# Optimization experiments

Hardware: AMD Instinct MI355X
Metric: run time of the kernel (lower is better)

Reference implementation:

```python
import jax, jax.numpy as jnp
import numpy as np

D_IN = 1024
D_OUT = 1024
NUM_HEADS = 16
HEAD_DIM = D_OUT // NUM_HEADS


def setup_inputs() -> dict:
    key = jax.random.key(0)
    ks = jax.random.split(key, 6)
    s = 0.02
    return {
        "x": jax.random.normal(ks[0], (4, 2048, D_IN), dtype=jnp.float32),
        "W_q": jax.random.normal(ks[1], (D_IN, D_OUT), dtype=jnp.float32) * s,
        "W_k": jax.random.normal(ks[2], (D_IN, D_OUT), dtype=jnp.float32) * s,
        "W_v": jax.random.normal(ks[3], (D_IN, D_OUT), dtype=jnp.float32) * s,
        "W_o": jax.random.normal(ks[4], (D_OUT, D_OUT), dtype=jnp.float32) * s,
        "b_o": jax.random.normal(ks[5], (D_OUT,), dtype=jnp.float32) * s,
    }


def reference(x, W_q, W_k, W_v, W_o, b_o):
    b, n, _ = x.shape
    # project and split heads: [b, h, n, d]
    q = (x @ W_q).reshape(b, n, NUM_HEADS, HEAD_DIM).transpose(0, 2, 1, 3)
    k = (x @ W_k).reshape(b, n, NUM_HEADS, HEAD_DIM).transpose(0, 2, 1, 3)
    v = (x @ W_v).reshape(b, n, NUM_HEADS, HEAD_DIM).transpose(0, 2, 1, 3)
    scores = jnp.einsum("bhqd,bhkd->bhqk", q, k)
    causal = jnp.tril(jnp.ones((n, n), dtype=bool))  # True = keep
    scores = jnp.where(causal, scores, -jnp.inf)
    attn = jax.nn.softmax(scores / np.sqrt(HEAD_DIM).astype(np.float32), axis=-1)
    ctx = jnp.einsum("bhqk,bhkd->bhqd", attn, v)
    ctx = ctx.transpose(0, 2, 1, 3).reshape(b, n, D_OUT)
    return ctx @ W_o + b_o
```

## Files before the change

### kernel.cpp

```cpp
#include <hip/hip_runtime.h>
#include <hip/hip_bf16.h>

#define NHEADS 16
#define HDIM 64
#define SEQ 2048
#define BATCH 4
#define DMODEL 1024
#define MTOT (BATCH * SEQ)

typedef short v8s __attribute__((ext_vector_type(8)));
typedef short v4s __attribute__((ext_vector_type(4)));
typedef float v4f __attribute__((ext_vector_type(4)));
typedef unsigned short u16;
typedef unsigned int u32;

__device__ __forceinline__ u16 f2bf(float f) {
    union { float f; unsigned u; } v; v.f = f;
    unsigned r = v.u + 0x7FFFu + ((v.u >> 16) & 1u);
    return (u16)(r >> 16);
}

__device__ __forceinline__ void g2l16(const u16* g, short* l) {
    __builtin_amdgcn_global_load_lds(
        (const __attribute__((address_space(1))) u32*)g,
        (__attribute__((address_space(3))) u32*)l, 16, 0, 0);
}

__global__ __launch_bounds__(256)
void xcvt(const float* __restrict__ x, u16* __restrict__ xb)
{
    size_t i = ((size_t)blockIdx.x * 256 + threadIdx.x) * 8;
    v4f a = *(const v4f*)&x[i];
    v4f b = *(const v4f*)&x[i + 4];
    v8s p;
#pragma unroll
    for (int e = 0; e < 4; ++e) p[e] = (short)f2bf(a[e]);
#pragma unroll
    for (int e = 0; e < 4; ++e) p[4 + e] = (short)f2bf(b[e]);
    *(v8s*)&xb[i] = p;
}

__global__ __launch_bounds__(256)
void transpose_w(const float* __restrict__ src, u16* __restrict__ dst)
{
    __shared__ __align__(8) short Ts[64 * 68];
    const int k0 = blockIdx.x * 64, n0 = blockIdx.y * 64;
    const int t = threadIdx.x;
    const int n4 = (t & 15) * 4, kl = t >> 4;
#pragma unroll
    for (int it = 0; it < 4; ++it) {
        int k = kl + 16 * it;
        v4f v = *(const v4f*)&src[(size_t)(k0 + k) * DMODEL + n0 + n4];
        v4s p;
#pragma unroll
        for (int e = 0; e < 4; ++e) p[e] = (short)f2bf(v[e]);
        *(v4s*)&Ts[k * 68 + n4] = p;
    }
    __syncthreads();
    const int nl = t >> 4, k4 = (t & 15) * 4;
#pragma unroll
    for (int it = 0; it < 4; ++it) {
        int n = nl + 16 * it;
        v4s o;
#pragma unroll
        for (int e = 0; e < 4; ++e) o[e] = Ts[(k4 + e) * 68 + n];
        *(v4s*)&dst[(size_t)(n0 + n) * DMODEL + k0 + k4] = o;
    }
}

__device__ __forceinline__ void qkv_epilogue(
    v4f (&acc)[4][4], int which, int n0, int m0, int wn, int wm,
    int l15, int quad, u16* Qb, u16* Kb, u16* Vt)
{
    if (which == 2) {
#pragma unroll
        for (int i = 0; i < 4; ++i)
#pragma unroll
            for (int j = 0; j < 4; ++j) {
                int col = n0 + wn + j * 16 + l15;
                int h = col >> 6, d = col & 63;
                int m = m0 + wm + i * 16 + quad * 4;
                int b = m >> 11, n = m & (SEQ - 1);
                v4s pv;
#pragma unroll
                for (int r = 0; r < 4; ++r) pv[r] = (short)f2bf(acc[i][j][r]);
                *(v4s*)&Vt[((size_t)(b * NHEADS + h) * HDIM + d) * SEQ + n] = pv;
            }
    } else {
        u16* Ob = (which == 0) ? Qb : Kb;
        const float scale = (which == 0) ? 0.125f : 1.0f;
#pragma unroll
        for (int i = 0; i < 4; ++i)
#pragma unroll
            for (int j = 0; j < 4; ++j) {
                int col = n0 + wn + j * 16 + l15;
                int h = col >> 6, d = col & 63;
#pragma unroll
                for (int r = 0; r < 4; ++r) {
                    int m = m0 + wm + i * 16 + quad * 4 + r;
                    int b = m >> 11, n = m & (SEQ - 1);
                    Ob[((size_t)(b * NHEADS + h) * SEQ + n) * HDIM + d] =
                        f2bf(acc[i][j][r] * scale);
                }
            }
    }
}

__global__ __launch_bounds__(256, 2)
void qkv_fast(const u16* __restrict__ xb, const u16* __restrict__ Wt,
              u16* __restrict__ Qb, u16* __restrict__ Kb, u16* __restrict__ Vt)
{
    __shared__ __align__(16) short As[128 * 32];
    __shared__ __align__(16) short Bs[128 * 32];

    const int which = blockIdx.z;
    const u16* W = Wt + (size_t)which * DMODEL * DMODEL;

    const int n0 = blockIdx.x * 128;
    const int m0 = blockIdx.y * 128;
    const int t = threadIdx.x;
    const int lane = t & 63;
    const int l15 = lane & 15;
    const int quad = lane >> 4;
    const int wave = t >> 6;
    const int wm = (wave >> 1) * 64;
    const int wn = (wave & 1) * 64;
    const int srow = t >> 2;
    const int sc8 = (t & 3) * 8;

    v4f acc[4][4];
#pragma unroll
    for (int i = 0; i < 4; ++i)
#pragma unroll
        for (int j = 0; j < 4; ++j) acc[i][j] = {0.f, 0.f, 0.f, 0.f};

    for (int k0 = 0; k0 < DMODEL; k0 += 32) {
        __syncthreads();
        g2l16(&xb[(size_t)(m0 + srow) * DMODEL + k0 + sc8], &As[srow * 32 + sc8]);
        g2l16(&xb[(size_t)(m0 + 64 + srow) * DMODEL + k0 + sc8],
              &As[(64 + srow) * 32 + sc8]);
        g2l16(&W[(size_t)(n0 + srow) * DMODEL + k0 + sc8], &Bs[srow * 32 + sc8]);
        g2l16(&W[(size_t)(n0 + 64 + srow) * DMODEL + k0 + sc8],
              &Bs[(64 + srow) * 32 + sc8]);
        __syncthreads();

        v8s af[4], bf[4];
#pragma unroll
        for (int i = 0; i < 4; ++i)
            af[i] = *(const v8s*)&As[(wm + i * 16 + l15) * 32 + quad * 8];
#pragma unroll
        for (int j = 0; j < 4; ++j)
            bf[j] = *(const v8s*)&Bs[(wn + j * 16 + l15) * 32 + quad * 8];
#pragma unroll
        for (int i = 0; i < 4; ++i)
#pragma unroll
            for (int j = 0; j < 4; ++j)
                acc[i][j] = __builtin_amdgcn_mfma_f32_16x16x32_bf16(
                    af[i], bf[j], acc[i][j], 0, 0, 0);
    }
    qkv_epilogue(acc, which, n0, m0, wn, wm, l15, quad, Qb, Kb, Vt);
}

__global__ __launch_bounds__(256, 2)
void qkv_slow(const float* __restrict__ x, const u16* __restrict__ Wt,
              u16* __restrict__ Qb, u16* __restrict__ Kb, u16* __restrict__ Vt)
{
    __shared__ __align__(16) short As[128 * 32];
    __shared__ __align__(16) short Bs[128 * 32];

    const int which = blockIdx.z;
    const u16* W = Wt + (size_t)which * DMODEL * DMODEL;

    const int n0 = blockIdx.x * 128;
    const int m0 = blockIdx.y * 128;
    const int t = threadIdx.x;
    const int lane = t & 63;
    const int l15 = lane & 15;
    const int quad = lane >> 4;
    const int wave = t >> 6;
    const int wm = (wave >> 1) * 64;
    const int wn = (wave & 1) * 64;
    const int srow = t >> 2;
    const int sc8 = (t & 3) * 8;

    v4f acc[4][4];
#pragma unroll
    for (int i = 0; i < 4; ++i)
#pragma unroll
        for (int j = 0; j < 4; ++j) acc[i][j] = {0.f, 0.f, 0.f, 0.f};

    for (int k0 = 0; k0 < DMODEL; k0 += 32) {
        __syncthreads();
        g2l16(&W[(size_t)(n0 + srow) * DMODEL + k0 + sc8], &Bs[srow * 32 + sc8]);
        g2l16(&W[(size_t)(n0 + 64 + srow) * DMODEL + k0 + sc8],
              &Bs[(64 + srow) * 32 + sc8]);
#pragma unroll
        for (int it = 0; it < 2; ++it) {
            int row = srow + 64 * it;
            const float* xp = &x[(size_t)(m0 + row) * DMODEL + k0 + sc8];
            v4f x0 = *(const v4f*)xp;
            v4f x1 = *(const v4f*)(xp + 4);
            v8s av;
#pragma unroll
            for (int e = 0; e < 4; ++e) av[e] = (short)f2bf(x0[e]);
#pragma unroll
            for (int e = 0; e < 4; ++e) av[4 + e] = (short)f2bf(x1[e]);
            *(v8s*)&As[row * 32 + sc8] = av;
        }
        __syncthreads();

        v8s af[4], bf[4];
#pragma unroll
        for (int i = 0; i < 4; ++i)
            af[i] = *(const v8s*)&As[(wm + i * 16 + l15) * 32 + quad * 8];
#pragma unroll
        for (int j = 0; j < 4; ++j)
            bf[j] = *(const v8s*)&Bs[(wn + j * 16 + l15) * 32 + quad * 8];
#pragma unroll
        for (int i = 0; i < 4; ++i)
#pragma unroll
            for (int j = 0; j < 4; ++j)
                acc[i][j] = __builtin_amdgcn_mfma_f32_16x16x32_bf16(
                    af[i], bf[j], acc[i][j], 0, 0, 0);
    }
    qkv_epilogue(acc, which, n0, m0, wn, wm, l15, quad, Qb, Kb, Vt);
}

#define KP 72

__global__ __launch_bounds__(256, 4)
void attn(const u16* __restrict__ Qb, const u16* __restrict__ Kb,
          const u16* __restrict__ Vt, u16* __restrict__ Cx)
{
    __shared__ __align__(16) short Ks[64 * KP];
    __shared__ __align__(16) short Vs[64 * KP];
    __shared__ __align__(16) short Ps[4 * 32 * KP];

    const int ell = blockIdx.x;
    const int xcd = ell & 7;
    const int rest = ell >> 3;
    const int p = rest & 7;
    const int bh = ((rest >> 3) << 3) | xcd;

    const int t = threadIdx.x;
    const int lane = t & 63;
    const int l15 = lane & 15;
    const int quad = lane >> 4;
    const int wave = t >> 6;

    const u16* Qh = Qb + (size_t)bh * SEQ * HDIM;
    const u16* Kh = Kb + (size_t)bh * SEQ * HDIM;
    const u16* Vh = Vt + (size_t)bh * HDIM * SEQ;
    short* Pw = &Ps[wave * 32 * KP];

    const int skey = t >> 2;
    const int sd = (t & 3) * 16;
    const int b = bh >> 4, h = bh & 15;

#pragma unroll 1
    for (int phase = 0; phase < 2; ++phase) {
        const int qt = phase ? (15 - p) : p;
        const int q0w = qt * 128 + wave * 32;
        const int kb_end = 2 * qt + 1;

        v8s qf[2][2];
#pragma unroll
        for (int qs = 0; qs < 2; ++qs)
#pragma unroll
            for (int hh = 0; hh < 2; ++hh)
                qf[qs][hh] = *(const v8s*)
                    &Qh[(size_t)(q0w + qs * 16 + l15) * HDIM + hh * 32 + quad * 8];

        v4f o[2][4];
        float ls[2][4];
#pragma unroll
        for (int qs = 0; qs < 2; ++qs) {
#pragma unroll
            for (int j = 0; j < 4; ++j) o[qs][j] = {0.f, 0.f, 0.f, 0.f};
#pragma unroll
            for (int r = 0; r < 4; ++r) ls[qs][r] = 0.f;
        }

        v8s pk0, pk1, pv0, pv1;
        {
            const u16* Kp = &Kh[(size_t)skey * HDIM + sd];
            pk0 = *(const v8s*)Kp; pk1 = *(const v8s*)(Kp + 8);
            const u16* Vp = &Vh[(size_t)skey * SEQ + sd];
            pv0 = *(const v8s*)Vp; pv1 = *(const v8s*)(Vp + 8);
        }

#pragma unroll 1
        for (int kb = 0; kb <= kb_end; ++kb) {
            __syncthreads();
            *(v8s*)&Ks[skey * KP + sd] = pk0;
            *(v8s*)&Ks[skey * KP + sd + 8] = pk1;
            *(v8s*)&Vs[skey * KP + sd] = pv0;
            *(v8s*)&Vs[skey * KP + sd + 8] = pv1;
            __syncthreads();

            if (kb < kb_end) {
                const u16* Kp = &Kh[(size_t)((kb + 1) * 64 + skey) * HDIM + sd];
                pk0 = *(const v8s*)Kp; pk1 = *(const v8s*)(Kp + 8);
                const u16* Vp = &Vh[(size_t)skey * SEQ + (kb + 1) * 64 + sd];
                pv0 = *(const v8s*)Vp; pv1 = *(const v8s*)(Vp + 8);
            }

            if ((kb * 64) <= q0w + 31) {
                const bool tail = (kb * 64 + 63) > q0w;
                v8s kf[4][2];
#pragma unroll
                for (int s = 0; s < 4; ++s)
#pragma unroll
                    for (int hh = 0; hh < 2; ++hh)
                        kf[s][hh] = *(const v8s*)
                            &Ks[(s * 16 + l15) * KP + hh * 32 + quad * 8];
#pragma unroll
                for (int qs = 0; qs < 2; ++qs)
#pragma unroll
                    for (int s = 0; s < 4; ++s) {
                        v4f a = {0.f, 0.f, 0.f, 0.f};
                        a = __builtin_amdgcn_mfma_f32_16x16x32_bf16(
                            qf[qs][0], kf[s][0], a, 0, 0, 0);
                        a = __builtin_amdgcn_mfma_f32_16x16x32_bf16(
                            qf[qs][1], kf[s][1], a, 0, 0, 0);
                        int key = kb * 64 + s * 16 + l15;
#pragma unroll
                        for (int r = 0; r < 4; ++r) {
                            int qrow = q0w + qs * 16 + quad * 4 + r;
                            float pe = (tail && key > qrow) ? 0.f : __expf(a[r]);
                            ls[qs][r] += pe;
                            Pw[(qs * 16 + quad * 4 + r) * KP + s * 16 + l15] =
                                (short)f2bf(pe);
                        }
                    }
                __asm__ volatile("s_waitcnt lgkmcnt(0)" ::: "memory");
#pragma unroll
                for (int ks = 0; ks < 2; ++ks) {
                    v8s pa0 = *(const v8s*)&Pw[l15 * KP + ks * 32 + quad * 8];
                    v8s pa1 = *(const v8s*)
                        &Pw[(16 + l15) * KP + ks * 32 + quad * 8];
#pragma unroll
                    for (int j = 0; j < 4; ++j) {
                        v8s vf = *(const v8s*)
                            &Vs[(j * 16 + l15) * KP + ks * 32 + quad * 8];
                        o[0][j] = __builtin_amdgcn_mfma_f32_16x16x32_bf16(
                            pa0, vf, o[0][j], 0, 0, 0);
                        o[1][j] = __builtin_amdgcn_mfma_f32_16x16x32_bf16(
                            pa1, vf, o[1][j], 0, 0, 0);
                    }
                }
            }
        }

#pragma unroll
        for (int qs = 0; qs < 2; ++qs)
#pragma unroll
            for (int r = 0; r < 4; ++r) {
                float v = ls[qs][r];
                v += __shfl_xor(v, 1, 64);
                v += __shfl_xor(v, 2, 64);
                v += __shfl_xor(v, 4, 64);
                v += __shfl_xor(v, 8, 64);
                ls[qs][r] = 1.f / v;
            }
#pragma unroll
        for (int qs = 0; qs < 2; ++qs)
#pragma unroll
            for (int j = 0; j < 4; ++j)
#pragma unroll
                for (int r = 0; r < 4; ++r) {
                    int qrow = q0w + qs * 16 + quad * 4 + r;
                    Cx[((size_t)(b * SEQ + qrow)) * DMODEL + h * HDIM +
                       j * 16 + l15] = f2bf(o[qs][j][r] * ls[qs][r]);
                }
    }
}

__global__ __launch_bounds__(256, 2)
void out_gemm(const u16* __restrict__ Cx, const u16* __restrict__ WoT,
              const float* __restrict__ bo, float* __restrict__ Y)
{
    __shared__ __align__(16) short As[128 * 32];
    __shared__ __align__(16) short Bs[128 * 32];

    const int n0 = blockIdx.x * 128;
    const int m0 = blockIdx.y * 128;
    const int t = threadIdx.x;
    const int lane = t & 63;
    const int l15 = lane & 15;
    const int quad = lane >> 4;
    const int wave = t >> 6;
    const int wm = (wave >> 1) * 64;
    const int wn = (wave & 1) * 64;
    const int srow = t >> 2;
    const int sc8 = (t & 3) * 8;

    v4f acc[4][4];
#pragma unroll
    for (int i = 0; i < 4; ++i)
#pragma unroll
        for (int j = 0; j < 4; ++j) acc[i][j] = {0.f, 0.f, 0.f, 0.f};

    for (int k0 = 0; k0 < DMODEL; k0 += 32) {
        __syncthreads();
        g2l16(&Cx[(size_t)(m0 + srow) * DMODEL + k0 + sc8], &As[srow * 32 + sc8]);
        g2l16(&Cx[(size_t)(m0 + 64 + srow) * DMODEL + k0 + sc8],
              &As[(64 + srow) * 32 + sc8]);
        g2l16(&WoT[(size_t)(n0 + srow) * DMODEL + k0 + sc8], &Bs[srow * 32 + sc8]);
        g2l16(&WoT[(size_t)(n0 + 64 + srow) * DMODEL + k0 + sc8],
              &Bs[(64 + srow) * 32 + sc8]);
        __syncthreads();

        v8s af[4], bf[4];
#pragma unroll
        for (int i = 0; i < 4; ++i)
            af[i] = *(const v8s*)&As[(wm + i * 16 + l15) * 32 + quad * 8];
#pragma unroll
        for (int j = 0; j < 4; ++j)
            bf[j] = *(const v8s*)&Bs[(wn + j * 16 + l15) * 32 + quad * 8];
#pragma unroll
        for (int i = 0; i < 4; ++i)
#pragma unroll
            for (int j = 0; j < 4; ++j)
                acc[i][j] = __builtin_amdgcn_mfma_f32_16x16x32_bf16(
                    af[i], bf[j], acc[i][j], 0, 0, 0);
    }

#pragma unroll
    for (int i = 0; i < 4; ++i)
#pragma unroll
        for (int j = 0; j < 4; ++j) {
            int col = n0 + wn + j * 16 + l15;
            float bias = bo[col];
#pragma unroll
            for (int r = 0; r < 4; ++r) {
                int m = m0 + wm + i * 16 + quad * 4 + r;
                Y[(size_t)m * DMODEL + col] = acc[i][j][r] + bias;
            }
        }
}

extern "C" void kernel_launch(void* const* d_in, const int* in_sizes, int n_in,
                              void* d_out, int out_size, void* d_ws,
                              size_t ws_size, hipStream_t stream)
{
    const float* x  = (const float*)d_in[0];
    const float* Wq = (const float*)d_in[1];
    const float* Wk = (const float*)d_in[2];
    const float* Wv = (const float*)d_in[3];
    const float* Wo = (const float*)d_in[4];
    const float* bo = (const float*)d_in[5];
    float* Y = (float*)d_out;

    const size_t per = (size_t)BATCH * NHEADS * SEQ * HDIM;
    const size_t wsz = (size_t)DMODEL * DMODEL;
    u16* base = (u16*)d_ws;

    if (ws_size >= (size_t)72 * 1024 * 1024) {
        u16* xb  = base;
        u16* Cx  = base;
        u16* Wt4 = base + per;
        u16* Qb  = base + per + 4 * wsz;
        u16* Kb  = Qb + per;
        u16* Vt  = Kb + per;

        xcvt<<<MTOT * DMODEL / (256 * 8), 256, 0, stream>>>(x, xb);
        transpose_w<<<dim3(16, 16), 256, 0, stream>>>(Wq, Wt4);
        transpose_w<<<dim3(16, 16), 256, 0, stream>>>(Wk, Wt4 + wsz);
        transpose_w<<<dim3(16, 16), 256, 0, stream>>>(Wv, Wt4 + 2 * wsz);
        transpose_w<<<dim3(16, 16), 256, 0, stream>>>(Wo, Wt4 + 3 * wsz);
        qkv_fast<<<dim3(DMODEL / 128, MTOT / 128, 3), 256, 0, stream>>>(
            xb, Wt4, Qb, Kb, Vt);
        attn<<<512, 256, 0, stream>>>(Qb, Kb, Vt, Cx);
        out_gemm<<<dim3(DMODEL / 128, MTOT / 128), 256, 0, stream>>>(
            Cx, Wt4 + 3 * wsz, bo, Y);
    } else {
        u16* Wt  = base;
        u16* Cx  = base;
        u16* Qb  = base + per;
        u16* WoT = base + per;
        u16* Kb  = base + 2 * per;
        u16* Vt  = base + 3 * per;

        transpose_w<<<dim3(16, 16), 256, 0, stream>>>(Wq, Wt);
        transpose_w<<<dim3(16, 16), 256, 0, stream>>>(Wk, Wt + wsz);
        transpose_w<<<dim3(16, 16), 256, 0, stream>>>(Wv, Wt + 2 * wsz);
        qkv_slow<<<dim3(DMODEL / 128, MTOT / 128, 3), 256, 0, stream>>>(
            x, Wt, Qb, Kb, Vt);
        attn<<<512, 256, 0, stream>>>(Qb, Kb, Vt, Cx);
        transpose_w<<<dim3(16, 16), 256, 0, stream>>>(Wo, WoT);
        out_gemm<<<dim3(DMODEL / 128, MTOT / 128), 256, 0, stream>>>(
            Cx, WoT, bo, Y);
    }
}
```

Baseline: 311.2 us.

## Halve attention query tile to 64 rows, double grid, fold log2e into Q scale

The attention kernel now gives each block a 64-query tile (16 rows per wave) instead of 128, and launches 1024 blocks with a reversed pairing of tiles so the causal work stays balanced. Only the diagonal key block is masked, and the per-wave skip branch goes away. The Q projection scale now includes log2(e), so exp2f replaces __expf, and P is rounded with a cheaper bf16 conversion. This is meant to raise parallelism and cut wasted causal work and exp cost. In exchange each K/V tile loaded into LDS is reused by fewer query rows, so K/V traffic and synchronisation per unit of compute go up.

```diff
diff --git a/kernel.cpp b/kernel.cpp
--- a/kernel.cpp
+++ b/kernel.cpp
@@ -19,6 +19,10 @@
     unsigned r = v.u + 0x7FFFu + ((v.u >> 16) & 1u);
     return (u16)(r >> 16);
 }
+__device__ __forceinline__ u16 f2bf_fast(float f) {
+    union { float f; unsigned u; } v; v.f = f;
+    return (u16)((v.u + 0x8000u) >> 16);
+}
 
 __device__ __forceinline__ void g2l16(const u16* g, short* l) {
     __builtin_amdgcn_global_load_lds(
@@ -67,6 +71,8 @@
         *(v4s*)&dst[(size_t)(n0 + n) * DMODEL + k0 + k4] = o;
     }
 }
+
+#define QSCALE (0.125f * 1.44269504088896f)
 
 __device__ __forceinline__ void qkv_epilogue(
     v4f (&acc)[4][4], int which, int n0, int m0, int wn, int wm,
@@ -88,7 +94,7 @@
             }
     } else {
         u16* Ob = (which == 0) ? Qb : Kb;
-        const float scale = (which == 0) ? 0.125f : 1.0f;
+        const float scale = (which == 0) ? QSCALE : 1.0f;
 #pragma unroll
         for (int i = 0; i < 4; ++i)
 #pragma unroll
@@ -234,13 +240,13 @@
 {
     __shared__ __align__(16) short Ks[64 * KP];
     __shared__ __align__(16) short Vs[64 * KP];
-    __shared__ __align__(16) short Ps[4 * 32 * KP];
+    __shared__ __align__(16) short Ps[4 * 16 * KP];
 
     const int ell = blockIdx.x;
     const int xcd = ell & 7;
     const int rest = ell >> 3;
-    const int p = rest & 7;
-    const int bh = ((rest >> 3) << 3) | xcd;
+    const int p = rest & 15;
+    const int bh = ((rest >> 4) << 3) | xcd;
 
     const int t = threadIdx.x;
     const int lane = t & 63;
@@ -251,7 +257,7 @@
     const u16* Qh = Qb + (size_t)bh * SEQ * HDIM;
     const u16* Kh = Kb + (size_t)bh * SEQ * HDIM;
     const u16* Vh = Vt + (size_t)bh * HDIM * SEQ;
-    short* Pw = &Ps[wave * 32 * KP];
+    short* Pw = &Ps[wave * 16 * KP];
 
     const int skey = t >> 2;
     const int sd = (t & 3) * 16;
@@ -259,27 +265,21 @@
 
 #pragma unroll 1
     for (int phase = 0; phase < 2; ++phase) {
-        const int qt = phase ? (15 - p) : p;
-        const int q0w = qt * 128 + wave * 32;
-        const int kb_end = 2 * qt + 1;
-
-        v8s qf[2][2];
-#pragma unroll
-        for (int qs = 0; qs < 2; ++qs)
-#pragma unroll
-            for (int hh = 0; hh < 2; ++hh)
-                qf[qs][hh] = *(const v8s*)
-                    &Qh[(size_t)(q0w + qs * 16 + l15) * HDIM + hh * 32 + quad * 8];
-
-        v4f o[2][4];
-        float ls[2][4];
-#pragma unroll
-        for (int qs = 0; qs < 2; ++qs) {
-#pragma unroll
-            for (int j = 0; j < 4; ++j) o[qs][j] = {0.f, 0.f, 0.f, 0.f};
-#pragma unroll
-            for (int r = 0; r < 4; ++r) ls[qs][r] = 0.f;
-        }
+        const int qt = phase ? p : (31 - p);
+        const int q0w = qt * 64 + wave * 16;
+
+        v8s qf[2];
+#pragma unroll
+        for (int hh = 0; hh < 2; ++hh)
+            qf[hh] = *(const v8s*)
+                &Qh[(size_t)(q0w + l15) * HDIM + hh * 32 + quad * 8];
+
+        v4f o[4];
+        float ls[4];
+#pragma unroll
+        for (int j = 0; j < 4; ++j) o[j] = {0.f, 0.f, 0.f, 0.f};
+#pragma unroll
+        for (int r = 0; r < 4; ++r) ls[r] = 0.f;
 
         v8s pk0, pk1, pv0, pv1;
         {
@@ -290,7 +290,7 @@
         }
 
 #pragma unroll 1
-        for (int kb = 0; kb <= kb_end; ++kb) {
+        for (int kb = 0; kb <= qt; ++kb) {
             __syncthreads();
             *(v8s*)&Ks[skey * KP + sd] = pk0;
             *(v8s*)&Ks[skey * KP + sd + 8] = pk1;
@@ -298,81 +298,61 @@
             *(v8s*)&Vs[skey * KP + sd + 8] = pv1;
             __syncthreads();
 
-            if (kb < kb_end) {
+            if (kb < qt) {
                 const u16* Kp = &Kh[(size_t)((kb + 1) * 64 + skey) * HDIM + sd];
                 pk0 = *(const v8s*)Kp; pk1 = *(const v8s*)(Kp + 8);
                 const u16* Vp = &Vh[(size_t)skey * SEQ + (kb + 1) * 64 + sd];
                 pv0 = *(const v8s*)Vp; pv1 = *(const v8s*)(Vp + 8);
             }
 
-            if ((kb * 64) <= q0w + 31) {
-                const bool tail = (kb * 64 + 63) > q0w;
-                v8s kf[4][2];
-#pragma unroll
-                for (int s = 0; s < 4; ++s)
-#pragma unroll
-                    for (int hh = 0; hh < 2; ++hh)
-                        kf[s][hh] = *(const v8s*)
-                            &Ks[(s * 16 + l15) * KP + hh * 32 + quad * 8];
-#pragma unroll
-                for (int qs = 0; qs < 2; ++qs)
-#pragma unroll
-                    for (int s = 0; s < 4; ++s) {
-                        v4f a = {0.f, 0.f, 0.f, 0.f};
-                        a = __builtin_amdgcn_mfma_f32_16x16x32_bf16(
-                            qf[qs][0], kf[s][0], a, 0, 0, 0);
-                        a = __builtin_amdgcn_mfma_f32_16x16x32_bf16(
-                            qf[qs][1], kf[s][1], a, 0, 0, 0);
-                        int key = kb * 64 + s * 16 + l15;
-#pragma unroll
-                        for (int r = 0; r < 4; ++r) {
-                            int qrow = q0w + qs * 16 + quad * 4 + r;
-                            float pe = (tail && key > qrow) ? 0.f : __expf(a[r]);
-                            ls[qs][r] += pe;
-                            Pw[(qs * 16 + quad * 4 + r) * KP + s * 16 + l15] =
-                                (short)f2bf(pe);
-                        }
-                    }
-                __asm__ volatile("s_waitcnt lgkmcnt(0)" ::: "memory");
-#pragma unroll
-                for (int ks = 0; ks < 2; ++ks) {
-                    v8s pa0 = *(const v8s*)&Pw[l15 * KP + ks * 32 + quad * 8];
-                    v8s pa1 = *(const v8s*)
-                        &Pw[(16 + l15) * KP + ks * 32 + quad * 8];
-#pragma unroll
-                    for (int j = 0; j < 4; ++j) {
-                        v8s vf = *(const v8s*)
-                            &Vs[(j * 16 + l15) * KP + ks * 32 + quad * 8];
-                        o[0][j] = __builtin_amdgcn_mfma_f32_16x16x32_bf16(
-                            pa0, vf, o[0][j], 0, 0, 0);
-                        o[1][j] = __builtin_amdgcn_mfma_f32_16x16x32_bf16(
-                            pa1, vf, o[1][j], 0, 0, 0);
-                    }
+            const bool tail = (kb == qt);
+#pragma unroll
+            for (int s = 0; s < 4; ++s) {
+                v8s kf0 = *(const v8s*)&Ks[(s * 16 + l15) * KP + quad * 8];
+                v8s kf1 = *(const v8s*)&Ks[(s * 16 + l15) * KP + 32 + quad * 8];
+                v4f a = {0.f, 0.f, 0.f, 0.f};
+                a = __builtin_amdgcn_mfma_f32_16x16x32_bf16(qf[0], kf0, a, 0, 0, 0);
+                a = __builtin_amdgcn_mfma_f32_16x16x32_bf16(qf[1], kf1, a, 0, 0, 0);
+                int key = kb * 64 + s * 16 + l15;
+#pragma unroll
+                for (int r = 0; r < 4; ++r) {
+                    int qrow = q0w + quad * 4 + r;
+                    float pe = (tail && key > qrow) ? 0.f : exp2f(a[r]);
+                    ls[r] += pe;
+                    Pw[(quad * 4 + r) * KP + s * 16 + l15] = (short)f2bf_fast(pe);
                 }
             }
+            __asm__ volatile("s_waitcnt lgkmcnt(0)" ::: "memory");
+#pragma unroll
+            for (int ks = 0; ks < 2; ++ks) {
+                v8s pa = *(const v8s*)&Pw[l15 * KP + ks * 32 + quad * 8];
+#pragma unroll
+                for (int j = 0; j < 4; ++j) {
+                    v8s vf = *(const v8s*)
+                        &Vs[(j * 16 + l15) * KP + ks * 32 + quad * 8];
+                    o[j] = __builtin_amdgcn_mfma_f32_16x16x32_bf16(
+                        pa, vf, o[j], 0, 0, 0);
+                }
+            }
         }
 
 #pragma unroll
-        for (int qs = 0; qs < 2; ++qs)
+        for (int r = 0; r < 4; ++r) {
+            float v = ls[r];
+            v += __shfl_xor(v, 1, 64);
+            v += __shfl_xor(v, 2, 64);
+            v += __shfl_xor(v, 4, 64);
+            v += __shfl_xor(v, 8, 64);
+            ls[r] = 1.f / v;
+        }
+#pragma unroll
+        for (int j = 0; j < 4; ++j)
 #pragma unroll
             for (int r = 0; r < 4; ++r) {
-                float v = ls[qs][r];
-                v += __shfl_xor(v, 1, 64);
-                v += __shfl_xor(v, 2, 64);
-                v += __shfl_xor(v, 4, 64);
-                v += __shfl_xor(v, 8, 64);
-                ls[qs][r] = 1.f / v;
-            }
-#pragma unroll
-        for (int qs = 0; qs < 2; ++qs)
-#pragma unroll
-            for (int j = 0; j < 4; ++j)
-#pragma unroll
-                for (int r = 0; r < 4; ++r) {
-                    int qrow = q0w + qs * 16 + quad * 4 + r;
-                    Cx[((size_t)(b * SEQ + qrow)) * DMODEL + h * HDIM +
-                       j * 16 + l15] = f2bf(o[qs][j][r] * ls[qs][r]);
-                }
+                int qrow = q0w + quad * 4 + r;
+                Cx[((size_t)(b * SEQ + qrow)) * DMODEL + h * HDIM + j * 16 + l15]
+                    = f2bf(o[j][r] * ls[r]);
+            }
     }
 }
 
@@ -471,7 +451,7 @@
         transpose_w<<<dim3(16, 16), 256, 0, stream>>>(Wo, Wt4 + 3 * wsz);
         qkv_fast<<<dim3(DMODEL / 128, MTOT / 128, 3), 256, 0, stream>>>(
             xb, Wt4, Qb, Kb, Vt);
-        attn<<<512, 256, 0, stream>>>(Qb, Kb, Vt, Cx);
+        attn<<<1024, 256, 0, stream>>>(Qb, Kb, Vt, Cx);
         out_gemm<<<dim3(DMODEL / 128, MTOT / 128), 256, 0, stream>>>(
             Cx, Wt4 + 3 * wsz, bo, Y);
     } else {
@@ -487,7 +467,7 @@
         transpose_w<<<dim3(16, 16), 256, 0, stream>>>(Wv, Wt + 2 * wsz);
         qkv_slow<<<dim3(DMODEL / 128, MTOT / 128, 3), 256, 0, stream>>>(
             x, Wt, Qb, Kb, Vt);
-        attn<<<512, 256, 0, stream>>>(Qb, Kb, Vt, Cx);
+        attn<<<1024, 256, 0, stream>>>(Qb, Kb, Vt, Cx);
         transpose_w<<<dim3(16, 16), 256, 0, stream>>>(Wo, WoT);
         out_gemm<<<dim3(DMODEL / 128, MTOT / 128), 256, 0, stream>>>(
             Cx, WoT, bo, Y);
```

Result: faster. 288.7 us (-7.2%).
